# Kernel tuning notes

Hardware: AMD Instinct MI355X
Metric: run time of the kernel (lower is better)

The kernel has to match this reference:

```python
import jax, jax.numpy as jnp
import numpy as np


def setup_inputs() -> dict:
    key = jax.random.key(0)
    k1, k2, k3, k4, k5 = jax.random.split(key, 5)
    B, Cin, D, H, W = 16, 16, 32, 32, 32
    Cout, Kd = 32, 3
    return {
        "x": jax.random.normal(k1, (B, Cin, D, H, W), dtype=jnp.float32),
        "weight": jax.random.normal(k2, (Cout, Cin, Kd, Kd, Kd), dtype=jnp.float32),
        "conv_bias": jax.random.normal(k3, (Cout,), dtype=jnp.float32),
        "scaling_factor": jax.random.normal(k4, (Cout, 1, 1, 1), dtype=jnp.float32),
        "bias_param": jax.random.normal(k5, (Cout, 1, 1, 1), dtype=jnp.float32),
    }


def reference(x, weight, conv_bias, scaling_factor, bias_param):
    # 3D valid conv, stride 1, NCDHW layout / OIDHW kernel
    y = jax.lax.conv_general_dilated(
        x, weight,
        window_strides=(1, 1, 1),
        padding="VALID",
        dimension_numbers=("NCDHW", "OIDHW", "NCDHW"),
    )
    # per-channel bias, scale, tanh, scale, sigmoid (broadcast over D,H,W)
    y = y + conv_bias[None, :, None, None, None]
    y = jnp.tanh(y * scaling_factor[None]) * bias_param[None]
    return jax.nn.sigmoid(y)
```

## Files before the change

kernel.cpp:

```cpp
#include <hip/hip_runtime.h>

#define NB    16
#define CIN   16
#define COUT  32
#define DIN   32
#define DOUT  30
#define XS_OFF 57344

typedef __attribute__((ext_vector_type(8)))  short  short8;
typedef __attribute__((ext_vector_type(16))) float  f32x16;

static __device__ __forceinline__ unsigned short f2bf_rne(float f) {
    unsigned int u = __builtin_bit_cast(unsigned int, f);
    u += 0x7fffu + ((u >> 16) & 1u);
    return (unsigned short)(u >> 16);
}
static __device__ __forceinline__ float bf2f(unsigned short s) {
    unsigned int u = ((unsigned int)s) << 16;
    return __builtin_bit_cast(float, u);
}

__global__ __launch_bounds__(256) void prep_kernel(const float* __restrict__ x,
                                                   const float* __restrict__ wgt,
                                                   char* __restrict__ ws) {
    const int bx  = blockIdx.x;
    const int tid = threadIdx.x;
    if (bx < 4096) {
        const int wy = tid >> 6, lane = tid & 63;
        const int rid = bx * 4 + wy;
        const int h = rid & 31, d = (rid >> 5) & 31, b = rid >> 10;
        const int w = lane >> 1, oc = lane & 1;
        const float* xp = x + ((((size_t)(b * 16 + oc * 8) * 32 + d) * 32 + h) * 32 + w);
        short8 vh, vl;
#pragma unroll
        for (int j = 0; j < 8; ++j) {
            float f = xp[j * 32768];
            unsigned short hb = f2bf_rne(f);
            vh[j] = (short)hb;
            vl[j] = (short)f2bf_rne(f - bf2f(hb));
        }
        char* row = ws + XS_OFF + (size_t)rid * 2048;
        *(short8*)(row + lane * 16)        = vh;
        *(short8*)(row + 1024 + lane * 16) = vl;
    } else if (tid < 64) {
        const int s = bx - 4096;
        const int l = tid;
        const int co = l & 31, ci0 = (l >> 5) * 8;
        short8 vh, vl;
#pragma unroll
        for (int j = 0; j < 8; ++j) {
            float f = wgt[co * (CIN * 27) + (ci0 + j) * 27 + s];
            unsigned short hb = f2bf_rne(f);
            vh[j] = (short)hb;
            vl[j] = (short)f2bf_rne(f - bf2f(hb));
        }
        ((short8*)ws)[s * 64 + l]           = vh;
        ((short8*)ws)[1728 + s * 64 + l]    = vl;
    }
}

__global__ __launch_bounds__(256) void conv_main(
    const char* __restrict__ ws,
    const float* __restrict__ cbias,
    const float* __restrict__ scal,
    const float* __restrict__ bpar,
    float* __restrict__ out)
{
    __shared__ __align__(16) short sx[24576];
    __shared__ float sp[96];

    const int htile = blockIdx.x;
    const int d2    = blockIdx.y;
    const int b     = blockIdx.z;
    const int tid  = threadIdx.x;
    const int wy   = tid >> 6;
    const int lane = tid & 63;

    if (tid < 32) {
        sp[tid]      = cbias[tid];
        sp[32 + tid] = scal[tid];
        sp[64 + tid] = bpar[tid];
    }

    const int h0 = htile * 4, d0 = d2 * 2;
    const char* xbase = ws + XS_OFF;
    const int psw = (lane ^ ((lane >> 3) & 7)) * 8;

#pragma unroll
    for (int r = wy * 12; r < wy * 12 + 12; ++r) {
        const int buf = r & 1, pr = r >> 1;
        const int p = pr / 6, row = pr - p * 6;
        int hin = h0 + row; if (hin > 31) hin = 31;
        const int rid = (b * 32 + d0 + p) * 32 + hin;
        const short8 v = *((const short8*)(xbase + (size_t)rid * 2048 + buf * 1024) + lane);
        *(short8*)(sx + (pr * 2 + buf) * 512 + psw) = v;
    }
    __syncthreads();

    const int h = h0 + wy;
    if (h >= DOUT) return;

    const int n  = lane & 31;
    const int oc = lane >> 5;
    int cofs[3];
#pragma unroll
    for (int kw = 0; kw < 3; ++kw) {
        int wc = n + kw; if (wc > 31) wc = 31;
        const int c = 2 * wc + oc;
        cofs[kw] = (c ^ ((c >> 3) & 7)) * 8;
    }

    f32x16 acc0, acc1;
#pragma unroll
    for (int i = 0; i < 16; ++i) { acc0[i] = 0.0f; acc1[i] = 0.0f; }

    const short8* wa = (const short8*)ws;
#pragma unroll
    for (int kh = 0; kh < 3; ++kh) {
        const int rowi = wy + kh;
#pragma unroll
        for (int kw = 0; kw < 3; ++kw) {
            short8 bh[4], bl[4];
#pragma unroll
            for (int p = 0; p < 4; ++p) {
                const short* slot = sx + ((p * 6 + rowi) * 2) * 512;
                bh[p] = *(const short8*)(slot + cofs[kw]);
                bl[p] = *(const short8*)(slot + 512 + cofs[kw]);
            }
#pragma unroll
            for (int kd = 0; kd < 3; ++kd) {
                const int s = kd * 9 + kh * 3 + kw;
                short8 ah = wa[s * 64 + lane];
                short8 al = wa[1728 + s * 64 + lane];
                acc0 = __builtin_amdgcn_mfma_f32_32x32x16_bf16(ah, bh[kd],     acc0, 0, 0, 0);
                acc1 = __builtin_amdgcn_mfma_f32_32x32x16_bf16(ah, bh[kd + 1], acc1, 0, 0, 0);
                acc0 = __builtin_amdgcn_mfma_f32_32x32x16_bf16(ah, bl[kd],     acc0, 0, 0, 0);
                acc1 = __builtin_amdgcn_mfma_f32_32x32x16_bf16(ah, bl[kd + 1], acc1, 0, 0, 0);
                acc0 = __builtin_amdgcn_mfma_f32_32x32x16_bf16(al, bh[kd],     acc0, 0, 0, 0);
                acc1 = __builtin_amdgcn_mfma_f32_32x32x16_bf16(al, bh[kd + 1], acc1, 0, 0, 0);
            }
        }
    }

    if (n < DOUT) {
        const int ob = b * (COUT * 27000) + h * 30 + n;
#pragma unroll
        for (int r = 0; r < 16; ++r) {
            const int co = (r & 3) + 8 * (r >> 2) + 4 * oc;
            float y0 = acc0[r] + sp[co];
            float t0 = y0 * sp[32 + co];
            float th0 = 1.0f - 2.0f / (__expf(2.0f * t0) + 1.0f);
            float z0 = th0 * sp[64 + co];
            out[ob + co * 27000 + d0 * 900] = 1.0f / (1.0f + __expf(-z0));

            float y1 = acc1[r] + sp[co];
            float t1 = y1 * sp[32 + co];
            float th1 = 1.0f - 2.0f / (__expf(2.0f * t1) + 1.0f);
            float z1 = th1 * sp[64 + co];
            out[ob + co * 27000 + (d0 + 1) * 900] = 1.0f / (1.0f + __expf(-z1));
        }
    }
}

__global__ __launch_bounds__(64) void repack_w_fb(const float* __restrict__ wgt,
                                                  short* __restrict__ ws) {
    const int s = blockIdx.x, l = threadIdx.x;
    const int co = l & 31, ci0 = (l >> 5) * 8;
    short8 vh, vl;
#pragma unroll
    for (int j = 0; j < 8; ++j) {
        float f = wgt[co * (CIN * 27) + (ci0 + j) * 27 + s];
        unsigned short hb = f2bf_rne(f);
        vh[j] = (short)hb;
        vl[j] = (short)f2bf_rne(f - bf2f(hb));
    }
    ((short8*)ws)[s * 64 + l]           = vh;
    ((short8*)ws)[27 * 64 + s * 64 + l] = vl;
}

__global__ __launch_bounds__(256) void conv3d_mfma_fb(
    const float* __restrict__ x, const short* __restrict__ wsA,
    const float* __restrict__ cbias, const float* __restrict__ scal,
    const float* __restrict__ bpar, float* __restrict__ out)
{
    __shared__ short sx[2 * 9216];
    __shared__ float sp[96];
    const int htile = blockIdx.x, d = blockIdx.y, b = blockIdx.z;
    const int tid = threadIdx.x, wy = tid >> 6, lane = tid & 63;
    if (tid < 32) { sp[tid] = cbias[tid]; sp[32 + tid] = scal[tid]; sp[64 + tid] = bpar[tid]; }
    const int h0 = htile * 4;
    const int xb = b * (CIN * DIN * DIN * DIN);
    for (int c = tid; c < 1152; c += 256) {
        const int hi8 = c & 1, r2 = c >> 1, w = r2 & 31, rr = r2 >> 5;
        const int dz = rr / 6, row = rr - dz * 6;
        int h_in = h0 + row; if (h_in > 31) h_in = 31;
        const int gbase = xb + (hi8 * 8) * (DIN * DIN * DIN) + (d + dz) * (DIN * DIN) + h_in * DIN + w;
        short8 vh, vl;
#pragma unroll
        for (int j = 0; j < 8; ++j) {
            float f = x[gbase + j * (DIN * DIN * DIN)];
            unsigned short hb = f2bf_rne(f);
            vh[j] = (short)hb; vl[j] = (short)f2bf_rne(f - bf2f(hb));
        }
        *(short8*)(sx + c * 8) = vh;
        *(short8*)(sx + 9216 + c * 8) = vl;
    }
    __syncthreads();
    const int h = h0 + wy;
    if (h >= DOUT) return;
    const int n = lane & 31, hi = lane >> 5;
    int wofs[3];
#pragma unroll
    for (int kw = 0; kw < 3; ++kw) { int wc = n + kw; if (wc > 31) wc = 31; wofs[kw] = wc * 16 + hi * 8; }
    f32x16 acc;
#pragma unroll
    for (int i = 0; i < 16; ++i) acc[i] = 0.0f;
    const short8* wa = (const short8*)wsA;
#pragma unroll
    for (int kd = 0; kd < 3; ++kd)
#pragma unroll
        for (int kh = 0; kh < 3; ++kh) {
            const int rbase = (kd * 6 + wy + kh) * (32 * 16);
#pragma unroll
            for (int kw = 0; kw < 3; ++kw) {
                const int s = kd * 9 + kh * 3 + kw;
                short8 ah = wa[s * 64 + lane];
                short8 al = wa[1728 + s * 64 + lane];
                short8 bh = *(const short8*)(sx + rbase + wofs[kw]);
                short8 bl = *(const short8*)(sx + 9216 + rbase + wofs[kw]);
                acc = __builtin_amdgcn_mfma_f32_32x32x16_bf16(ah, bh, acc, 0, 0, 0);
                acc = __builtin_amdgcn_mfma_f32_32x32x16_bf16(ah, bl, acc, 0, 0, 0);
                acc = __builtin_amdgcn_mfma_f32_32x32x16_bf16(al, bh, acc, 0, 0, 0);
            }
        }
    if (n < DOUT) {
        const int obase = b * (COUT * 27000) + d * 900 + h * 30 + n;
#pragma unroll
        for (int r = 0; r < 16; ++r) {
            const int co = (r & 3) + 8 * (r >> 2) + 4 * hi;
            float y = acc[r] + sp[co];
            float t = y * sp[32 + co];
            float th = 1.0f - 2.0f / (__expf(2.0f * t) + 1.0f);
            float z = th * sp[64 + co];
            out[obase + co * 27000] = 1.0f / (1.0f + __expf(-z));
        }
    }
}

__global__ __launch_bounds__(256) void conv3d_direct_fb(
    const float* __restrict__ x, const float* __restrict__ wgt,
    const float* __restrict__ cbias, const float* __restrict__ scal,
    const float* __restrict__ bpar, float* __restrict__ out)
{
    __shared__ float sw[CIN * 27];
    const int bx = blockIdx.x, co = blockIdx.y, b = blockIdx.z;
    const int tid = threadIdx.y * 32 + threadIdx.x;
    for (int i = tid; i < CIN * 27; i += 256) sw[i] = wgt[co * (CIN * 27) + i];
    __syncthreads();
    const float bias = cbias[co], s = scal[co], bp = bpar[co];
    const int dt = bx & 7, ht = bx >> 3;
    const int d0 = dt * 4, h = ht * 8 + threadIdx.y, w = threadIdx.x;
    if (w >= DOUT || h >= DOUT) return;
    int rowoff[6];
#pragma unroll
    for (int dz = 0; dz < 6; ++dz) { int dd = d0 + dz; if (dd > 31) dd = 31; rowoff[dz] = dd * 1024; }
    float acc[4] = {0.f, 0.f, 0.f, 0.f};
    const int xb = b * (CIN * 32768);
    for (int ci = 0; ci < CIN; ++ci) {
        const int cioff = xb + ci * 32768;
        const float* swc = &sw[ci * 27];
#pragma unroll
        for (int kh = 0; kh < 3; ++kh) {
            const int hbase = cioff + (h + kh) * DIN + w;
#pragma unroll
            for (int kw = 0; kw < 3; ++kw) {
                float xv[6];
#pragma unroll
                for (int dz = 0; dz < 6; ++dz) xv[dz] = x[hbase + kw + rowoff[dz]];
#pragma unroll
                for (int kd = 0; kd < 3; ++kd) {
                    const float wv = swc[(kd * 3 + kh) * 3 + kw];
#pragma unroll
                    for (int dd = 0; dd < 4; ++dd) acc[dd] = fmaf(xv[dd + kd], wv, acc[dd]);
                }
            }
        }
    }
    const int obase = (b * COUT + co) * 27000 + h * 30 + w;
#pragma unroll
    for (int dd = 0; dd < 4; ++dd) {
        const int d = d0 + dd;
        if (d < DOUT) {
            float y = acc[dd] + bias;
            float t = y * s;
            float th = 1.0f - 2.0f / (__expf(2.0f * t) + 1.0f);
            float z = th * bp;
            out[obase + d * 900] = 1.0f / (1.0f + __expf(-z));
        }
    }
}

extern "C" void kernel_launch(void* const* d_in, const int* in_sizes, int n_in,
                              void* d_out, int out_size, void* d_ws, size_t ws_size,
                              hipStream_t stream) {
    const float* x     = (const float*)d_in[0];
    const float* wgt   = (const float*)d_in[1];
    const float* cbias = (const float*)d_in[2];
    const float* scal  = (const float*)d_in[3];
    const float* bpar  = (const float*)d_in[4];
    float* out = (float*)d_out;

    const size_t need_full = (size_t)XS_OFF + (size_t)16384 * 2048;
    if (ws_size >= need_full) {
        char* ws = (char*)d_ws;
        hipLaunchKernelGGL(prep_kernel, dim3(4096 + 27), dim3(256), 0, stream, x, wgt, ws);
        hipLaunchKernelGGL(conv_main, dim3(8, 15, NB), dim3(256), 0, stream,
                           ws, cbias, scal, bpar, out);
    } else if (ws_size >= 55296) {
        short* ws = (short*)d_ws;
        hipLaunchKernelGGL(repack_w_fb, dim3(27), dim3(64), 0, stream, wgt, ws);
        hipLaunchKernelGGL(conv3d_mfma_fb, dim3(8, DOUT, NB), dim3(256), 0, stream,
                           x, ws, cbias, scal, bpar, out);
    } else {
        hipLaunchKernelGGL(conv3d_direct_fb, dim3(32, COUT, NB), dim3(32, 8), 0, stream,
                           x, wgt, cbias, scal, bpar, out);
    }
}
```

Measured before the change: 146.8 us.

## Fuse input/weight bf16 split into a single large-LDS conv kernel

```diff
diff --git a/kernel.cpp b/kernel.cpp
--- a/kernel.cpp
+++ b/kernel.cpp
@@ -5,7 +5,6 @@
 #define COUT  32
 #define DIN   32
 #define DOUT  30
-#define XS_OFF 57344
 
 typedef __attribute__((ext_vector_type(8)))  short  short8;
 typedef __attribute__((ext_vector_type(16))) float  f32x16;
@@ -19,6 +18,141 @@
     unsigned int u = ((unsigned int)s) << 16;
     return __builtin_bit_cast(float, u);
 }
+
+#define SWH 0
+#define SWL 13824
+#define SXH 27648
+#define SXL 46080
+#define SP_BYTES 129024
+#define LDS_BYTES 129408
+
+__global__ __launch_bounds__(512, 1) void conv_one(
+    const float* __restrict__ x,
+    const float* __restrict__ wgt,
+    const float* __restrict__ cbias,
+    const float* __restrict__ scal,
+    const float* __restrict__ bpar,
+    float* __restrict__ out)
+{
+    extern __shared__ __align__(16) char smem_raw[];
+    short* sm = (short*)smem_raw;
+    float* sp = (float*)(smem_raw + SP_BYTES);
+
+    const int htile = blockIdx.x;
+    const int dtile = blockIdx.y;
+    const int b     = blockIdx.z;
+    const int tid  = threadIdx.x;
+    const int wy   = tid >> 6;
+    const int lane = tid & 63;
+
+    if (tid < 32) {
+        sp[tid]      = cbias[tid];
+        sp[32 + tid] = scal[tid];
+        sp[64 + tid] = bpar[tid];
+    }
+
+    for (int i = tid; i < 1728; i += 512) {
+        const int s = i >> 6, l = i & 63;
+        const int co = l & 31, ci0 = (l >> 5) * 8;
+        short8 vh, vl;
+#pragma unroll
+        for (int j = 0; j < 8; ++j) {
+            float f = wgt[co * (CIN * 27) + (ci0 + j) * 27 + s];
+            unsigned short hb = f2bf_rne(f);
+            vh[j] = (short)hb;
+            vl[j] = (short)f2bf_rne(f - bf2f(hb));
+        }
+        *(short8*)(sm + SWH + i * 8) = vh;
+        *(short8*)(sm + SWL + i * 8) = vl;
+    }
+
+    const int h0 = htile * 4, d0 = dtile * 4;
+    for (int c = tid; c < 2304; c += 512) {
+        const int oc = c & 1, t = c >> 1;
+        const int w = t & 31, pr = t >> 5;
+        const int p = pr / 6, r = pr - p * 6;
+        int hin = h0 + r; if (hin > 31) hin = 31;
+        int din = d0 + p; if (din > 31) din = 31;
+        const float* xp = x + ((((b * 16 + oc * 8) * 32 + din) * 32 + hin) * 32 + w);
+        short8 vh, vl;
+#pragma unroll
+        for (int j = 0; j < 8; ++j) {
+            float f = xp[j * 32768];
+            unsigned short hb = f2bf_rne(f);
+            vh[j] = (short)hb;
+            vl[j] = (short)f2bf_rne(f - bf2f(hb));
+        }
+        *(short8*)(sm + SXH + pr * 512 + w * 16 + oc * 8) = vh;
+        *(short8*)(sm + SXL + pr * 512 + w * 16 + oc * 8) = vl;
+    }
+    __syncthreads();
+
+    const int hrow = wy & 3, dg = (wy >> 2) * 2;
+    const int h  = h0 + hrow;
+    const int da = d0 + dg;
+    if (h >= DOUT || da >= DOUT) return;
+
+    const int n   = lane & 31;
+    const int oc2 = lane >> 5;
+    int cofs[3];
+#pragma unroll
+    for (int kw = 0; kw < 3; ++kw) {
+        int wc = n + kw; if (wc > 31) wc = 31;
+        cofs[kw] = wc * 16 + oc2 * 8;
+    }
+
+    f32x16 acc0, acc1;
+#pragma unroll
+    for (int i = 0; i < 16; ++i) { acc0[i] = 0.0f; acc1[i] = 0.0f; }
+
+#pragma unroll
+    for (int kh = 0; kh < 3; ++kh) {
+        const int rowi = hrow + kh;
+#pragma unroll
+        for (int kw = 0; kw < 3; ++kw) {
+            short8 bh[4], bl[4];
+#pragma unroll
+            for (int q = 0; q < 4; ++q) {
+                const int slot = (dg + q) * 6 + rowi;
+                bh[q] = *(const short8*)(sm + SXH + slot * 512 + cofs[kw]);
+                bl[q] = *(const short8*)(sm + SXL + slot * 512 + cofs[kw]);
+            }
+#pragma unroll
+            for (int kd = 0; kd < 3; ++kd) {
+                const int s = kd * 9 + kh * 3 + kw;
+                short8 ah = *(const short8*)(sm + SWH + (s * 64 + lane) * 8);
+                short8 al = *(const short8*)(sm + SWL + (s * 64 + lane) * 8);
+                acc0 = __builtin_amdgcn_mfma_f32_32x32x16_bf16(ah, bh[kd],     acc0, 0, 0, 0);
+                acc1 = __builtin_amdgcn_mfma_f32_32x32x16_bf16(ah, bh[kd + 1], acc1, 0, 0, 0);
+                acc0 = __builtin_amdgcn_mfma_f32_32x32x16_bf16(ah, bl[kd],     acc0, 0, 0, 0);
+                acc1 = __builtin_amdgcn_mfma_f32_32x32x16_bf16(ah, bl[kd + 1], acc1, 0, 0, 0);
+                acc0 = __builtin_amdgcn_mfma_f32_32x32x16_bf16(al, bh[kd],     acc0, 0, 0, 0);
+                acc1 = __builtin_amdgcn_mfma_f32_32x32x16_bf16(al, bh[kd + 1], acc1, 0, 0, 0);
+            }
+        }
+    }
+
+    if (n < DOUT) {
+        const int ob = b * (COUT * 27000) + h * 30 + n;
+#pragma unroll
+        for (int r = 0; r < 16; ++r) {
+            const int co = (r & 3) + 8 * (r >> 2) + 4 * oc2;
+            float y0 = acc0[r] + sp[co];
+            float t0 = y0 * sp[32 + co];
+            float th0 = 1.0f - 2.0f / (__expf(2.0f * t0) + 1.0f);
+            float z0 = th0 * sp[64 + co];
+            out[ob + co * 27000 + da * 900] = 1.0f / (1.0f + __expf(-z0));
+
+            float y1 = acc1[r] + sp[co];
+            float t1 = y1 * sp[32 + co];
+            float th1 = 1.0f - 2.0f / (__expf(2.0f * t1) + 1.0f);
+            float z1 = th1 * sp[64 + co];
+            out[ob + co * 27000 + (da + 1) * 900] = 1.0f / (1.0f + __expf(-z1));
+        }
+    }
+}
+
+#define XS_OFF 57344
 
 __global__ __launch_bounds__(256) void prep_kernel(const float* __restrict__ x,
                                                    const float* __restrict__ wgt,
@@ -54,8 +188,8 @@
             vh[j] = (short)hb;
             vl[j] = (short)f2bf_rne(f - bf2f(hb));
         }
-        ((short8*)ws)[s * 64 + l]           = vh;
-        ((short8*)ws)[1728 + s * 64 + l]    = vl;
+        ((short8*)ws)[s * 64 + l]        = vh;
+        ((short8*)ws)[1728 + s * 64 + l] = vl;
     }
 }
 
@@ -68,24 +202,12 @@
 {
     __shared__ __align__(16) short sx[24576];
     __shared__ float sp[96];
-
-    const int htile = blockIdx.x;
-    const int d2    = blockIdx.y;
-    const int b     = blockIdx.z;
-    const int tid  = threadIdx.x;
-    const int wy   = tid >> 6;
-    const int lane = tid & 63;
-
-    if (tid < 32) {
-        sp[tid]      = cbias[tid];
-        sp[32 + tid] = scal[tid];
-        sp[64 + tid] = bpar[tid];
-    }
-
+    const int htile = blockIdx.x, d2 = blockIdx.y, b = blockIdx.z;
+    const int tid = threadIdx.x, wy = tid >> 6, lane = tid & 63;
+    if (tid < 32) { sp[tid] = cbias[tid]; sp[32 + tid] = scal[tid]; sp[64 + tid] = bpar[tid]; }
     const int h0 = htile * 4, d0 = d2 * 2;
     const char* xbase = ws + XS_OFF;
-    const int psw = (lane ^ ((lane >> 3) & 7)) * 8;
-
+    const int psw = lane * 8;
 #pragma unroll
     for (int r = wy * 12; r < wy * 12 + 12; ++r) {
         const int buf = r & 1, pr = r >> 1;
@@ -96,24 +218,18 @@
         *(short8*)(sx + (pr * 2 + buf) * 512 + psw) = v;
     }
     __syncthreads();
-
     const int h = h0 + wy;
     if (h >= DOUT) return;
-
-    const int n  = lane & 31;
-    const int oc = lane >> 5;
+    const int n = lane & 31, oc = lane >> 5;
     int cofs[3];
 #pragma unroll
     for (int kw = 0; kw < 3; ++kw) {
         int wc = n + kw; if (wc > 31) wc = 31;
-        const int c = 2 * wc + oc;
-        cofs[kw] = (c ^ ((c >> 3) & 7)) * 8;
-    }
-
+        cofs[kw] = (2 * wc + oc) * 8;
+    }
     f32x16 acc0, acc1;
 #pragma unroll
     for (int i = 0; i < 16; ++i) { acc0[i] = 0.0f; acc1[i] = 0.0f; }
-
     const short8* wa = (const short8*)ws;
 #pragma unroll
     for (int kh = 0; kh < 3; ++kh) {
@@ -141,7 +257,6 @@
             }
         }
     }
-
     if (n < DOUT) {
         const int ob = b * (COUT * 27000) + h * 30 + n;
 #pragma unroll
@@ -152,97 +267,11 @@
             float th0 = 1.0f - 2.0f / (__expf(2.0f * t0) + 1.0f);
             float z0 = th0 * sp[64 + co];
             out[ob + co * 27000 + d0 * 900] = 1.0f / (1.0f + __expf(-z0));
-
             float y1 = acc1[r] + sp[co];
             float t1 = y1 * sp[32 + co];
             float th1 = 1.0f - 2.0f / (__expf(2.0f * t1) + 1.0f);
             float z1 = th1 * sp[64 + co];
             out[ob + co * 27000 + (d0 + 1) * 900] = 1.0f / (1.0f + __expf(-z1));
-        }
-    }
-}
-
-__global__ __launch_bounds__(64) void repack_w_fb(const float* __restrict__ wgt,
-                                                  short* __restrict__ ws) {
-    const int s = blockIdx.x, l = threadIdx.x;
-    const int co = l & 31, ci0 = (l >> 5) * 8;
-    short8 vh, vl;
-#pragma unroll
-    for (int j = 0; j < 8; ++j) {
-        float f = wgt[co * (CIN * 27) + (ci0 + j) * 27 + s];
-        unsigned short hb = f2bf_rne(f);
-        vh[j] = (short)hb;
-        vl[j] = (short)f2bf_rne(f - bf2f(hb));
-    }
-    ((short8*)ws)[s * 64 + l]           = vh;
-    ((short8*)ws)[27 * 64 + s * 64 + l] = vl;
-}
-
-__global__ __launch_bounds__(256) void conv3d_mfma_fb(
-    const float* __restrict__ x, const short* __restrict__ wsA,
-    const float* __restrict__ cbias, const float* __restrict__ scal,
-    const float* __restrict__ bpar, float* __restrict__ out)
-{
-    __shared__ short sx[2 * 9216];
-    __shared__ float sp[96];
-    const int htile = blockIdx.x, d = blockIdx.y, b = blockIdx.z;
-    const int tid = threadIdx.x, wy = tid >> 6, lane = tid & 63;
-    if (tid < 32) { sp[tid] = cbias[tid]; sp[32 + tid] = scal[tid]; sp[64 + tid] = bpar[tid]; }
-    const int h0 = htile * 4;
-    const int xb = b * (CIN * DIN * DIN * DIN);
-    for (int c = tid; c < 1152; c += 256) {
-        const int hi8 = c & 1, r2 = c >> 1, w = r2 & 31, rr = r2 >> 5;
-        const int dz = rr / 6, row = rr - dz * 6;
-        int h_in = h0 + row; if (h_in > 31) h_in = 31;
-        const int gbase = xb + (hi8 * 8) * (DIN * DIN * DIN) + (d + dz) * (DIN * DIN) + h_in * DIN + w;
-        short8 vh, vl;
-#pragma unroll
-        for (int j = 0; j < 8; ++j) {
-            float f = x[gbase + j * (DIN * DIN * DIN)];
-            unsigned short hb = f2bf_rne(f);
-            vh[j] = (short)hb; vl[j] = (short)f2bf_rne(f - bf2f(hb));
-        }
-        *(short8*)(sx + c * 8) = vh;
-        *(short8*)(sx + 9216 + c * 8) = vl;
-    }
-    __syncthreads();
-    const int h = h0 + wy;
-    if (h >= DOUT) return;
-    const int n = lane & 31, hi = lane >> 5;
-    int wofs[3];
-#pragma unroll
-    for (int kw = 0; kw < 3; ++kw) { int wc = n + kw; if (wc > 31) wc = 31; wofs[kw] = wc * 16 + hi * 8; }
-    f32x16 acc;
-#pragma unroll
-    for (int i = 0; i < 16; ++i) acc[i] = 0.0f;
-    const short8* wa = (const short8*)wsA;
-#pragma unroll
-    for (int kd = 0; kd < 3; ++kd)
-#pragma unroll
-        for (int kh = 0; kh < 3; ++kh) {
-            const int rbase = (kd * 6 + wy + kh) * (32 * 16);
-#pragma unroll
-            for (int kw = 0; kw < 3; ++kw) {
-                const int s = kd * 9 + kh * 3 + kw;
-                short8 ah = wa[s * 64 + lane];
-                short8 al = wa[1728 + s * 64 + lane];
-                short8 bh = *(const short8*)(sx + rbase + wofs[kw]);
-                short8 bl = *(const short8*)(sx + 9216 + rbase + wofs[kw]);
-                acc = __builtin_amdgcn_mfma_f32_32x32x16_bf16(ah, bh, acc, 0, 0, 0);
-                acc = __builtin_amdgcn_mfma_f32_32x32x16_bf16(ah, bl, acc, 0, 0, 0);
-                acc = __builtin_amdgcn_mfma_f32_32x32x16_bf16(al, bh, acc, 0, 0, 0);
-            }
-        }
-    if (n < DOUT) {
-        const int obase = b * (COUT * 27000) + d * 900 + h * 30 + n;
-#pragma unroll
-        for (int r = 0; r < 16; ++r) {
-            const int co = (r & 3) + 8 * (r >> 2) + 4 * hi;
-            float y = acc[r] + sp[co];
-            float t = y * sp[32 + co];
-            float th = 1.0f - 2.0f / (__expf(2.0f * t) + 1.0f);
-            float z = th * sp[64 + co];
-            out[obase + co * 27000] = 1.0f / (1.0f + __expf(-z));
         }
     }
 }
@@ -310,17 +339,20 @@
     const float* bpar  = (const float*)d_in[4];
     float* out = (float*)d_out;
 
+    hipError_t aerr = hipFuncSetAttribute((const void*)conv_one,
+                                          hipFuncAttributeMaxDynamicSharedMemorySize,
+                                          LDS_BYTES);
+    if (aerr == hipSuccess) {
+        hipLaunchKernelGGL(conv_one, dim3(8, 8, NB), dim3(512), LDS_BYTES, stream,
+                           x, wgt, cbias, scal, bpar, out);
+        if (hipGetLastError() == hipSuccess) return;
+    }
     const size_t need_full = (size_t)XS_OFF + (size_t)16384 * 2048;
     if (ws_size >= need_full) {
         char* ws = (char*)d_ws;
         hipLaunchKernelGGL(prep_kernel, dim3(4096 + 27), dim3(256), 0, stream, x, wgt, ws);
         hipLaunchKernelGGL(conv_main, dim3(8, 15, NB), dim3(256), 0, stream,
                            ws, cbias, scal, bpar, out);
-    } else if (ws_size >= 55296) {
-        short* ws = (short*)d_ws;
-        hipLaunchKernelGGL(repack_w_fb, dim3(27), dim3(64), 0, stream, wgt, ws);
-        hipLaunchKernelGGL(conv3d_mfma_fb, dim3(8, DOUT, NB), dim3(256), 0, stream,
-                           x, ws, cbias, scal, bpar, out);
     } else {
         hipLaunchKernelGGL(conv3d_direct_fb, dim3(32, COUT, NB), dim3(32, 8), 0, stream,
                            x, wgt, cbias, scal, bpar, out);
```

New measurement: 180.5 us. 23.0% more time.
